# Optimization experiments

Measured on AMD Instinct MI355X. Metric: run time of the kernel, lower is better.

The kernel has to match this reference:

```python
import jax, jax.numpy as jnp
import numpy as np

ALPHA = 0.2          # LeakyReLU negative slope
NEG_INF = -9e15      # standard GAT masking constant


def gat_layer(h, adj_mask, W, a_src, a_dst):
    # h: [N, D], adj_mask: [N, N] bool
    Wh = h @ W                                  # [N, D]
    e = (Wh @ a_src)[:, None] + (Wh @ a_dst)[None, :]  # [N, N]
    e = jax.nn.leaky_relu(e, negative_slope=ALPHA)
    e = jnp.where(adj_mask, e, NEG_INF)
    attn = jax.nn.softmax(e, axis=-1)           # [N, N]
    return jax.nn.relu(attn @ Wh)               # PlainGCN applies ReLU


def setup_inputs() -> dict:
    key = jax.random.key(0)
    ks = jax.random.split(key, 8)
    N, D = 8192, 256
    x = jax.random.normal(ks[0], (N, D), dtype=jnp.float32)
    adj = jax.random.randint(ks[1], (N, N), 0, 2, dtype=jnp.int32)
    s = 1.0 / np.sqrt(D)
    W1 = jax.random.normal(ks[2], (D, D), dtype=jnp.float32) * s
    a1_src = jax.random.normal(ks[3], (D,), dtype=jnp.float32) * s
    a1_dst = jax.random.normal(ks[4], (D,), dtype=jnp.float32) * s
    W2 = jax.random.normal(ks[5], (D, D), dtype=jnp.float32) * s
    a2_src = jax.random.normal(ks[6], (D,), dtype=jnp.float32) * s
    a2_dst = jax.random.normal(ks[7], (D,), dtype=jnp.float32) * s
    return {"x": x, "adj": adj, "W1": W1, "a1_src": a1_src, "a1_dst": a1_dst,
            "W2": W2, "a2_src": a2_src, "a2_dst": a2_dst}


def reference(x, adj, W1, a1_src, a1_dst, W2, a2_src, a2_dst):
    adj_mask = adj > 0
    h = gat_layer(x, adj_mask, W1, a1_src, a1_dst)
    h = gat_layer(h, adj_mask, W2, a2_src, a2_dst)
    return h
```

## Files before the change

kernel.cpp:

```cpp
#include <hip/hip_runtime.h>
#include <cstdint>
#include <cstddef>


#define ALPHA 0.2f
#define NN 8192
#define DD 256

typedef __attribute__((ext_vector_type(8))) short short8;
typedef __attribute__((ext_vector_type(4))) float f32x4;
typedef __attribute__((ext_vector_type(2))) _Float16 half2v;
typedef __attribute__((ext_vector_type(8))) __fp16 h8;

__device__ __forceinline__ unsigned pk_f16(float a, float b) {
    return __builtin_bit_cast(unsigned, __builtin_amdgcn_cvt_pkrtz(a, b));
}

__device__ __forceinline__ int sbit(uint32_t x, int o) {
    return ((int)(x << (31 - o))) >> 31;
}

__device__ __forceinline__ uint32_t hmerge(uint32_t hi, uint32_t lo) {
#if __has_builtin(__builtin_amdgcn_perm)
    return __builtin_amdgcn_perm(hi, lo, 0x07060100u);
#else
    return (hi & 0xFFFF0000u) | (lo & 0x0000FFFFu);
#endif
}

__device__ __forceinline__ half2v pkmax(half2v a, half2v b) {
#if __has_builtin(__builtin_elementwise_max)
    return __builtin_elementwise_max(a, b);
#else
    half2v r;
    asm("v_pk_max_f16 %0, %1, %2" : "=v"(r) : "v"(a), "v"(b));
    return r;
#endif
}

__device__ __forceinline__ f32x4 mfma_f16(uint4 a, short8 b, f32x4 c) {
    return __builtin_amdgcn_mfma_f32_16x16x32_f16(__builtin_bit_cast(h8, a),
                                                  __builtin_bit_cast(h8, b), c, 0, 0, 0);
}


__device__ __forceinline__ void packbits_dev(const int* __restrict__ adj,
                                             uint64_t* __restrict__ bits,
                                             int row, int lane) {
    const int* rowp = adj + (size_t)row * NN;
    uint64_t* dst = bits + (size_t)row * 128;
    for (int it = 0; it < 16; it++) {
        const int* p = rowp + it * 512;
        int a0 = p[lane];
        int a1 = p[64 + lane];
        int a2 = p[128 + lane];
        int a3 = p[192 + lane];
        int a4 = p[256 + lane];
        int a5 = p[320 + lane];
        int a6 = p[384 + lane];
        int a7 = p[448 + lane];
        uint64_t m0 = __ballot(a0 != 0);
        uint64_t m1 = __ballot(a1 != 0);
        uint64_t m2 = __ballot(a2 != 0);
        uint64_t m3 = __ballot(a3 != 0);
        uint64_t m4 = __ballot(a4 != 0);
        uint64_t m5 = __ballot(a5 != 0);
        uint64_t m6 = __ballot(a6 != 0);
        uint64_t m7 = __ballot(a7 != 0);
        if (lane == 0) {
            dst[it * 8 + 0] = m0; dst[it * 8 + 1] = m1;
            dst[it * 8 + 2] = m2; dst[it * 8 + 3] = m3;
            dst[it * 8 + 4] = m4; dst[it * 8 + 5] = m5;
            dst[it * 8 + 6] = m6; dst[it * 8 + 7] = m7;
        }
    }
}

__device__ __forceinline__ void transp_dev(const uint32_t* __restrict__ bits32,
                                           uint32_t* __restrict__ bitsT,
                                           int job, unsigned char* smem, int t) {
    uint32_t (*tile)[65] = (uint32_t (*)[65])smem;
    const int i0 = (job >> 2) * 64;
    const int w0 = (job & 3) * 64;
#pragma unroll
    for (int p = 0; p < 4; p++) {
        int r = (t >> 4) + 16 * p;
        int c4 = (t & 15) * 4;
        uint4 v = *(const uint4*)(bits32 + (size_t)(i0 + r) * 256 + w0 + c4);
        tile[r][c4 + 0] = v.x; tile[r][c4 + 1] = v.y;
        tile[r][c4 + 2] = v.z; tile[r][c4 + 3] = v.w;
    }
    __syncthreads();
#pragma unroll
    for (int p = 0; p < 4; p++) {
        int wr = (t >> 4) + 16 * p;
        int i4 = (t & 15) * 4;
        uint4 o = {tile[i4][wr], tile[i4 + 1][wr], tile[i4 + 2][wr], tile[i4 + 3][wr]};
        *(uint4*)(bitsT + (size_t)(w0 + wr) * NN + i0 + i4) = o;
    }
}

__device__ __forceinline__ void gemm_dev(const float* __restrict__ A,
                                         const float* __restrict__ B,
                                         unsigned short* __restrict__ Bpack,
                                         const float* __restrict__ a_src,
                                         const float* __restrict__ a_dst,
                                         float* __restrict__ s4,
                                         float* __restrict__ dd4,
                                         int job, unsigned char* smem, int t) {
    float (*At)[36] = (float (*)[36])smem;
    float2 (*Bs)[32] = (float2 (*)[32])(smem + 4608);
    const int m0 = (job >> 2) * 32;
    const int cq = job & 3;
    const int r0 = (t >> 5) * 4;
    const int cl = t & 31;
    float acc[4][2];
#pragma unroll
    for (int i = 0; i < 4; i++) { acc[i][0] = 0.f; acc[i][1] = 0.f; }

    for (int k0 = 0; k0 < DD; k0 += 32) {
        {
            int row = t >> 3, kq = t & 7;
            float4 v = *(const float4*)(A + (size_t)(m0 + row) * DD + k0 + kq * 4);
            At[kq * 4 + 0][row] = v.x; At[kq * 4 + 1][row] = v.y;
            At[kq * 4 + 2][row] = v.z; At[kq * 4 + 3][row] = v.w;
        }
#pragma unroll
        for (int l2 = 0; l2 < 2; l2++) {
            int fi = l2 * 256 + t;
            int br = fi >> 4, bc4 = fi & 15;
            float4 v = *(const float4*)(B + (size_t)(k0 + br) * DD + cq * 64 + bc4 * 4);
            Bs[br][bc4 * 2] = {v.x, v.y};
            Bs[br][bc4 * 2 + 1] = {v.z, v.w};
        }
        __syncthreads();
#pragma unroll
        for (int k = 0; k < 32; k++) {
            float4 a0 = *(const float4*)&At[k][r0];
            float2 b = Bs[k][cl];
            float av[4] = {a0.x, a0.y, a0.z, a0.w};
#pragma unroll
            for (int i = 0; i < 4; i++) {
                acc[i][0] += av[i] * b.x;
                acc[i][1] += av[i] * b.y;
            }
        }
        __syncthreads();
    }

    const int jt = m0 >> 5;
    const int lq = ((r0 >> 3) & 3) * 16;
    const int i8 = r0 & 4;
#pragma unroll
    for (int cc = 0; cc < 2; cc++) {
        int c = cq * 64 + cl * 2 + cc;
        int ct = c >> 4;
        int lane = lq + (c & 15);
        uint2 pk;
        pk.x = pk_f16(acc[0][cc], acc[1][cc]);
        pk.y = pk_f16(acc[2][cc], acc[3][cc]);
        *(uint2*)(Bpack + ((size_t)(jt * 16 + ct) * 64 + lane) * 8 + i8) = pk;
    }

    const int c0 = cq * 64 + cl * 2;
    float as0 = a_src[c0], as1 = a_src[c0 + 1];
    float ad0 = a_dst[c0], ad1 = a_dst[c0 + 1];
    float ps[4], pd[4];
#pragma unroll
    for (int i = 0; i < 4; i++) {
        ps[i] = acc[i][0] * as0 + acc[i][1] * as1;
        pd[i] = acc[i][0] * ad0 + acc[i][1] * ad1;
    }
#pragma unroll
    for (int off = 16; off; off >>= 1) {
#pragma unroll
        for (int i = 0; i < 4; i++) {
            ps[i] += __shfl_xor(ps[i], off);
            pd[i] += __shfl_xor(pd[i], off);
        }
    }
    if (cl == 0) {
#pragma unroll
        for (int i = 0; i < 4; i++) {
            s4[(size_t)cq * NN + m0 + r0 + i] = ps[i];
            dd4[(size_t)cq * NN + m0 + r0 + i] = pd[i];
        }
    }
}

__device__ __forceinline__ void fhgen_dev(const float* __restrict__ s4,
                                          const float* __restrict__ dd4,
                                          float* __restrict__ s,
                                          uint32_t* __restrict__ FF,
                                          uint32_t* __restrict__ HH,
                                          float* __restrict__ dmax32,
                                          int job, float* sred, int t) {
    const int i = job * 256 + t;
    float ssum = (s4[i] + s4[i + NN]) + (s4[i + 2 * NN] + s4[i + 3 * NN]);
    float dsum = (dd4[i] + dd4[i + NN]) + (dd4[i + 2 * NN] + dd4[i + 3 * NN]);
    s[i] = ssum;
    float F = __expf(dsum);
    float H = __expf(ALPHA * dsum);
    float Fn = __shfl_xor(F, 1);
    float Hn = __shfl_xor(H, 1);
    if ((i & 1) == 0) {
        FF[i >> 1] = pk_f16(F, Fn);
        HH[i >> 1] = pk_f16(H, Hn);
    }
    float bm = dsum;
#pragma unroll
    for (int off = 32; off; off >>= 1) bm = fmaxf(bm, __shfl_xor(bm, off));
    const int wave = t >> 6, lane = t & 63;
    if (lane == 0) sred[wave] = bm;
    __syncthreads();
    if (t == 0) dmax32[job] = fmaxf(fmaxf(sred[0], sred[1]), fmaxf(sred[2], sred[3]));
}


__global__ __launch_bounds__(256) void mega1(const float* __restrict__ A,
                                             const float* __restrict__ W,
                                             unsigned short* __restrict__ Bpack,
                                             const float* __restrict__ a_src,
                                             const float* __restrict__ a_dst,
                                             float* __restrict__ s4,
                                             float* __restrict__ dd4,
                                             const int* __restrict__ adj,
                                             uint64_t* __restrict__ bits) {
    __shared__ __align__(16) unsigned char smem[12800];
    const int bx = blockIdx.x;
    const int t = threadIdx.x;
    const int sel = bx % 3;
    const int base = bx / 3;
    if (sel == 0) {
        gemm_dev(A, W, Bpack, a_src, a_dst, s4, dd4, base, smem, t);
    } else {
        const int row = base * 8 + (sel - 1) * 4 + (t >> 6);
        packbits_dev(adj, bits, row, t & 63);
    }
}

__global__ __launch_bounds__(256) void megaB(const uint32_t* __restrict__ bits32,
                                             uint32_t* __restrict__ bitsT,
                                             const float* __restrict__ s4,
                                             const float* __restrict__ dd4,
                                             float* __restrict__ s,
                                             uint32_t* __restrict__ FF,
                                             uint32_t* __restrict__ HH,
                                             float* __restrict__ dmax32) {
    __shared__ __align__(16) unsigned char smem[16640];
    const int bx = blockIdx.x;
    const int t = threadIdx.x;
    if (bx < 512) {
        transp_dev(bits32, bitsT, bx, smem, t);
    } else {
        fhgen_dev(s4, dd4, s, FF, HH, dmax32, bx - 512, (float*)smem, t);
    }
}

__global__ __launch_bounds__(256) void k_gemm(const float* A, const float* W,
                                              unsigned short* Bpack,
                                              const float* a_src, const float* a_dst,
                                              float* s4, float* dd4) {
    __shared__ __align__(16) unsigned char smem[12800];
    gemm_dev(A, W, Bpack, a_src, a_dst, s4, dd4, blockIdx.x, smem, threadIdx.x);
}
__global__ __launch_bounds__(256) void k_fhgen(const float* __restrict__ s4,
                                               const float* __restrict__ dd4,
                                               float* __restrict__ s,
                                               uint32_t* __restrict__ FF,
                                               uint32_t* __restrict__ HH,
                                               float* __restrict__ dmax32) {
    __shared__ float sred[4];
    fhgen_dev(s4, dd4, s, FF, HH, dmax32, blockIdx.x, sred, threadIdx.x);
}

__global__ __launch_bounds__(256) void epgen(const float* __restrict__ s,
                                             const float* __restrict__ dmax32,
                                             float* __restrict__ Ep,
                                             float* __restrict__ Gp) {
    __shared__ float sm;
    const int t = threadIdx.x;
    if (t == 0) {
        float m = dmax32[0];
#pragma unroll
        for (int k = 1; k < 32; k++) m = fmaxf(m, dmax32[k]);
        sm = m;
    }
    __syncthreads();
    const float dmax = sm;
    const int i = blockIdx.x * 256 + t;
    float si = s[i];
    float e = si + dmax;
    float m = e >= 0.f ? e : ALPHA * e;
    Ep[i] = 256.0f * __expf(si - m);
    Gp[i] = 256.0f * __expf(ALPHA * si - m);
}

__global__ __launch_bounds__(256, 4) void pv_mfma(const unsigned short* __restrict__ Bpack,
                                                  const uint32_t* __restrict__ bitsT,
                                                  const uint32_t* __restrict__ FF,
                                                  const uint32_t* __restrict__ HH,
                                                  const float* __restrict__ Ep,
                                                  const float* __restrict__ Gp,
                                                  float* __restrict__ pout,
                                                  float* __restrict__ rsum) {
    __shared__ __align__(16) uint4 pb[2][256];
    __shared__ __align__(16) uint32_t sFF[512];
    __shared__ __align__(16) uint32_t sHH[512];
    const int t = threadIdx.x;
    const int w = t >> 6, l = t & 63;
    const int bx = blockIdx.x;
    const int ks = bx & 7;
    const int i0 = (bx >> 3) * 64;
    const int kbase = ks * 32;

    const int rl16 = l & 15;
    const int ko = (l >> 4) * 8;
    const int fo = ko >> 1;
    const int rw = i0 + 16 * w + rl16;
    const _Float16 eph = (_Float16)Ep[rw];
    const _Float16 gph = (_Float16)Gp[rw];
    const half2v ep2 = {eph, eph};
    const half2v gp2 = {gph, gph};

    const unsigned short* bb = Bpack + ((size_t)(w * 4) * 64 + l) * 8;
    const uint32_t* btb = bitsT + rw;

    if (t < 128) {
        ((uint4*)sFF)[t] = *(const uint4*)(FF + kbase * 16 + t * 4);
    } else {
        ((uint4*)sHH)[t - 128] = *(const uint4*)(HH + kbase * 16 + (t - 128) * 4);
    }

    f32x4 acc[4][4];
#pragma unroll
    for (int i = 0; i < 4; i++)
#pragma unroll
        for (int q = 0; q < 4; q++) acc[i][q] = (f32x4){0.f, 0.f, 0.f, 0.f};
    float rsv = 0.f;

    auto build = [&](int jl, uint32_t bw) -> uint4 {
        uint4 fw = *(const uint4*)(sFF + jl * 16 + fo);
        uint4 hw = *(const uint4*)(sHH + jl * 16 + fo);
        const uint32_t fwa[4] = {fw.x, fw.y, fw.z, fw.w};
        const uint32_t hwa[4] = {hw.x, hw.y, hw.z, hw.w};
        const uint32_t wl = bw >> ko;
        uint32_t au[4];
#pragma unroll
        for (int p = 0; p < 4; p++) {
            half2v f2 = __builtin_bit_cast(half2v, fwa[p]);
            half2v h2 = __builtin_bit_cast(half2v, hwa[p]);
            half2v pm = ep2 * f2;
            half2v pa = gp2 * h2;
            half2v px = pkmax(pm, pa);
            uint32_t mlo = (uint32_t)sbit(wl, 2 * p);
            uint32_t mhi = (uint32_t)sbit(wl, 2 * p + 1);
            au[p] = __builtin_bit_cast(uint32_t, px) & hmerge(mhi, mlo);
        }
        half2v s01 = __builtin_bit_cast(half2v, au[0]) + __builtin_bit_cast(half2v, au[1]);
        half2v s23 = __builtin_bit_cast(half2v, au[2]) + __builtin_bit_cast(half2v, au[3]);
        half2v sp = s01 + s23;
        rsv += (float)sp.x + (float)sp.y;
        return (uint4){au[0], au[1], au[2], au[3]};
    };

    uint32_t bwc = btb[(size_t)kbase * NN];
    __syncthreads();

    uint4 aucur = build(0, bwc);
    pb[0][w * 64 + l] = aucur;
    uint32_t bwn = btb[(size_t)(kbase + 1) * NN];

    for (int jl = 0; jl < 32; jl++) {
        const int par = jl & 1;
        const unsigned short* bp = bb + (size_t)(kbase + jl) * 8192;
        short8 B0 = *(const short8*)(bp);
        short8 B1 = *(const short8*)(bp + 512);
        short8 B2 = *(const short8*)(bp + 1024);
        short8 B3 = *(const short8*)(bp + 1536);

        __syncthreads();

#pragma unroll
        for (int f = 0; f < 4; f++) {
            uint4 af;
            if (f == w) af = aucur;
            else        af = pb[par][f * 64 + l];
            acc[f][0] = mfma_f16(af, B0, acc[f][0]);
            acc[f][1] = mfma_f16(af, B1, acc[f][1]);
            acc[f][2] = mfma_f16(af, B2, acc[f][2]);
            acc[f][3] = mfma_f16(af, B3, acc[f][3]);
        }

        if (jl < 31) {
            uint4 an = build(jl + 1, bwn);
            pb[par ^ 1][w * 64 + l] = an;
            aucur = an;
            if (jl < 30) bwn = btb[(size_t)(kbase + jl + 2) * NN];
        }
    }

    rsv += __shfl_xor(rsv, 16);
    rsv += __shfl_xor(rsv, 32);
    if (l < 16) rsum[(size_t)ks * NN + rw] = rsv;

    float* outp = pout + (size_t)ks * NN * DD;
#pragma unroll
    for (int f = 0; f < 4; f++) {
        const int orow = i0 + 16 * f + (l >> 4) * 4;
#pragma unroll
        for (int q = 0; q < 4; q++) {
            const int ocol = w * 64 + q * 16 + rl16;
#pragma unroll
            for (int r = 0; r < 4; r++)
                outp[(size_t)(orow + r) * DD + ocol] = acc[f][q][r];
        }
    }
}

__global__ __launch_bounds__(256) void combine8(const float* __restrict__ p,
                                                const float* __restrict__ rsum,
                                                float* __restrict__ out) {
    const size_t S = (size_t)NN * DD / 4;
    size_t idx = (size_t)blockIdx.x * 256 + threadIdx.x;
    const int row = (int)(idx >> 6);
    float rs = (rsum[row] + rsum[row + NN]) + (rsum[row + 2 * NN] + rsum[row + 3 * NN])
             + (rsum[row + 4 * NN] + rsum[row + 5 * NN])
             + (rsum[row + 6 * NN] + rsum[row + 7 * NN]);
    const float inv = 1.0f / rs;
    float4 a0 = ((const float4*)p)[idx];
    float4 a1 = ((const float4*)p)[idx + S];
    float4 a2 = ((const float4*)p)[idx + 2 * S];
    float4 a3 = ((const float4*)p)[idx + 3 * S];
    float4 a4 = ((const float4*)p)[idx + 4 * S];
    float4 a5 = ((const float4*)p)[idx + 5 * S];
    float4 a6 = ((const float4*)p)[idx + 6 * S];
    float4 a7 = ((const float4*)p)[idx + 7 * S];
    float4 o;
    o.x = fmaxf((((a0.x + a1.x) + (a2.x + a3.x)) + ((a4.x + a5.x) + (a6.x + a7.x))) * inv, 0.f);
    o.y = fmaxf((((a0.y + a1.y) + (a2.y + a3.y)) + ((a4.y + a5.y) + (a6.y + a7.y))) * inv, 0.f);
    o.z = fmaxf((((a0.z + a1.z) + (a2.z + a3.z)) + ((a4.z + a5.z) + (a6.z + a7.z))) * inv, 0.f);
    o.w = fmaxf((((a0.w + a1.w) + (a2.w + a3.w)) + ((a4.w + a5.w) + (a6.w + a7.w))) * inv, 0.f);
    ((float4*)out)[idx] = o;
}

extern "C" void kernel_launch(void* const* d_in, const int* in_sizes, int n_in,
                              void* d_out, int out_size, void* d_ws, size_t ws_size,
                              hipStream_t stream) {
    const float* x   = (const float*)d_in[0];
    const int* adj   = (const int*)d_in[1];
    const float* W1  = (const float*)d_in[2];
    const float* a1s = (const float*)d_in[3];
    const float* a1d = (const float*)d_in[4];
    const float* W2  = (const float*)d_in[5];
    const float* a2s = (const float*)d_in[6];
    const float* a2d = (const float*)d_in[7];
    float* out = (float*)d_out;

    char* ws = (char*)d_ws;
    const size_t MB = 1024ull * 1024ull;
    uint64_t*       bits  = (uint64_t*)(ws + 8 * MB);
    uint32_t*       bits32= (uint32_t*)bits;
    uint32_t*       bitsT = (uint32_t*)(ws + 16 * MB);
    float*          sArr  = (float*)(ws + 24 * MB);
    float*          EpA   = sArr + NN;
    float*          GpA   = sArr + 2 * NN;
    float*          s4    = sArr + 3 * NN;
    float*          dd4   = sArr + 7 * NN;
    float*          rsumA = sArr + 11 * NN;
    uint32_t*       FFA   = (uint32_t*)(sArr + 19 * NN);
    uint32_t*       HHA   = FFA + NN / 2;
    float*          dmax32= sArr + 20 * NN;
    unsigned short* Bpack = (unsigned short*)(ws + 25 * MB);
    float*          pout  = (float*)(ws + 32 * MB);

    mega1<<<dim3(3072), dim3(256), 0, stream>>>(x, W1, Bpack, a1s, a1d, s4, dd4,
                                                adj, bits);
    megaB<<<dim3(544), dim3(256), 0, stream>>>(bits32, bitsT, s4, dd4, sArr,
                                               FFA, HHA, dmax32);
    epgen<<<dim3(32), dim3(256), 0, stream>>>(sArr, dmax32, EpA, GpA);
    pv_mfma<<<dim3(1024), dim3(256), 0, stream>>>(Bpack, bitsT, FFA, HHA, EpA, GpA,
                                                  pout, rsumA);
    combine8<<<dim3(2048), dim3(256), 0, stream>>>(pout, rsumA, out);

    k_gemm<<<dim3(1024), dim3(256), 0, stream>>>(out, W2, Bpack, a2s, a2d, s4, dd4);
    k_fhgen<<<dim3(32), dim3(256), 0, stream>>>(s4, dd4, sArr, FFA, HHA, dmax32);
    epgen<<<dim3(32), dim3(256), 0, stream>>>(sArr, dmax32, EpA, GpA);
    pv_mfma<<<dim3(1024), dim3(256), 0, stream>>>(Bpack, bitsT, FFA, HHA, EpA, GpA,
                                                  pout, rsumA);
    combine8<<<dim3(2048), dim3(256), 0, stream>>>(pout, rsumA, out);
}
```

Baseline: 517.7 us.

## Fold epgen into pv_mfma and halve the split-K partitions from eight to four

Removes the separate epgen kernel by having every pv_mfma wave reduce dmax32 with shuffles and compute its row's Ep/Gp scale factors inline. The split-K factor over the 256 column blocks drops from 8 to 4, so each block runs 64 iterations and there are 512 blocks. This halves the partial-output traffic written by pv_mfma and read by combine4, and removes two launches. The cost is half as many blocks, which lowers occupancy and parallelism, and a longer serial loop per block.

```diff
diff --git a/kernel.cpp b/kernel.cpp
--- a/kernel.cpp
+++ b/kernel.cpp
@@ -274,63 +274,45 @@
     fhgen_dev(s4, dd4, s, FF, HH, dmax32, blockIdx.x, sred, threadIdx.x);
 }
 
-__global__ __launch_bounds__(256) void epgen(const float* __restrict__ s,
-                                             const float* __restrict__ dmax32,
-                                             float* __restrict__ Ep,
-                                             float* __restrict__ Gp) {
-    __shared__ float sm;
-    const int t = threadIdx.x;
-    if (t == 0) {
-        float m = dmax32[0];
-#pragma unroll
-        for (int k = 1; k < 32; k++) m = fmaxf(m, dmax32[k]);
-        sm = m;
-    }
-    __syncthreads();
-    const float dmax = sm;
-    const int i = blockIdx.x * 256 + t;
-    float si = s[i];
-    float e = si + dmax;
-    float m = e >= 0.f ? e : ALPHA * e;
-    Ep[i] = 256.0f * __expf(si - m);
-    Gp[i] = 256.0f * __expf(ALPHA * si - m);
-}
-
 __global__ __launch_bounds__(256, 4) void pv_mfma(const unsigned short* __restrict__ Bpack,
                                                   const uint32_t* __restrict__ bitsT,
                                                   const uint32_t* __restrict__ FF,
                                                   const uint32_t* __restrict__ HH,
-                                                  const float* __restrict__ Ep,
-                                                  const float* __restrict__ Gp,
+                                                  const float* __restrict__ s,
+                                                  const float* __restrict__ dmax32,
                                                   float* __restrict__ pout,
                                                   float* __restrict__ rsum) {
     __shared__ __align__(16) uint4 pb[2][256];
-    __shared__ __align__(16) uint32_t sFF[512];
-    __shared__ __align__(16) uint32_t sHH[512];
+    __shared__ __align__(16) uint32_t sFF[1024];
+    __shared__ __align__(16) uint32_t sHH[1024];
     const int t = threadIdx.x;
     const int w = t >> 6, l = t & 63;
     const int bx = blockIdx.x;
-    const int ks = bx & 7;
-    const int i0 = (bx >> 3) * 64;
-    const int kbase = ks * 32;
+    const int ks = bx & 3;
+    const int i0 = (bx >> 2) * 64;
+    const int kbase = ks * 64;
 
     const int rl16 = l & 15;
     const int ko = (l >> 4) * 8;
     const int fo = ko >> 1;
     const int rw = i0 + 16 * w + rl16;
-    const _Float16 eph = (_Float16)Ep[rw];
-    const _Float16 gph = (_Float16)Gp[rw];
-    const half2v ep2 = {eph, eph};
-    const half2v gp2 = {gph, gph};
+
+    float dm = (l < 32) ? dmax32[l] : -3.0e38f;
+#pragma unroll
+    for (int off = 32; off; off >>= 1) dm = fmaxf(dm, __shfl_xor(dm, off));
+    const float si = s[rw];
+    const float e0 = si + dm;
+    const float m = e0 >= 0.f ? e0 : ALPHA * e0;
+    const float Eps = 256.0f * __expf(si - m);
+    const float Gps = 256.0f * __expf(ALPHA * si - m);
+    const half2v ep2 = {(_Float16)Eps, (_Float16)Eps};
+    const half2v gp2 = {(_Float16)Gps, (_Float16)Gps};
 
     const unsigned short* bb = Bpack + ((size_t)(w * 4) * 64 + l) * 8;
     const uint32_t* btb = bitsT + rw;
 
-    if (t < 128) {
-        ((uint4*)sFF)[t] = *(const uint4*)(FF + kbase * 16 + t * 4);
-    } else {
-        ((uint4*)sHH)[t - 128] = *(const uint4*)(HH + kbase * 16 + (t - 128) * 4);
-    }
+    ((uint4*)sFF)[t] = *(const uint4*)(FF + kbase * 16 + t * 4);
+    ((uint4*)sHH)[t] = *(const uint4*)(HH + kbase * 16 + t * 4);
 
     f32x4 acc[4][4];
 #pragma unroll
@@ -371,7 +353,7 @@
     pb[0][w * 64 + l] = aucur;
     uint32_t bwn = btb[(size_t)(kbase + 1) * NN];
 
-    for (int jl = 0; jl < 32; jl++) {
+    for (int jl = 0; jl < 64; jl++) {
         const int par = jl & 1;
         const unsigned short* bp = bb + (size_t)(kbase + jl) * 8192;
         short8 B0 = *(const short8*)(bp);
@@ -392,11 +374,11 @@
             acc[f][3] = mfma_f16(af, B3, acc[f][3]);
         }
 
-        if (jl < 31) {
+        if (jl < 63) {
             uint4 an = build(jl + 1, bwn);
             pb[par ^ 1][w * 64 + l] = an;
             aucur = an;
-            if (jl < 30) bwn = btb[(size_t)(kbase + jl + 2) * NN];
+            if (jl < 62) bwn = btb[(size_t)(kbase + jl + 2) * NN];
         }
     }
 
@@ -418,29 +400,23 @@
     }
 }
 
-__global__ __launch_bounds__(256) void combine8(const float* __restrict__ p,
+__global__ __launch_bounds__(256) void combine4(const float* __restrict__ p,
                                                 const float* __restrict__ rsum,
                                                 float* __restrict__ out) {
     const size_t S = (size_t)NN * DD / 4;
     size_t idx = (size_t)blockIdx.x * 256 + threadIdx.x;
     const int row = (int)(idx >> 6);
-    float rs = (rsum[row] + rsum[row + NN]) + (rsum[row + 2 * NN] + rsum[row + 3 * NN])
-             + (rsum[row + 4 * NN] + rsum[row + 5 * NN])
-             + (rsum[row + 6 * NN] + rsum[row + 7 * NN]);
+    float rs = (rsum[row] + rsum[row + NN]) + (rsum[row + 2 * NN] + rsum[row + 3 * NN]);
     const float inv = 1.0f / rs;
     float4 a0 = ((const float4*)p)[idx];
     float4 a1 = ((const float4*)p)[idx + S];
     float4 a2 = ((const float4*)p)[idx + 2 * S];
     float4 a3 = ((const float4*)p)[idx + 3 * S];
-    float4 a4 = ((const float4*)p)[idx + 4 * S];
-    float4 a5 = ((const float4*)p)[idx + 5 * S];
-    float4 a6 = ((const float4*)p)[idx + 6 * S];
-    float4 a7 = ((const float4*)p)[idx + 7 * S];
     float4 o;
-    o.x = fmaxf((((a0.x + a1.x) + (a2.x + a3.x)) + ((a4.x + a5.x) + (a6.x + a7.x))) * inv, 0.f);
-    o.y = fmaxf((((a0.y + a1.y) + (a2.y + a3.y)) + ((a4.y + a5.y) + (a6.y + a7.y))) * inv, 0.f);
-    o.z = fmaxf((((a0.z + a1.z) + (a2.z + a3.z)) + ((a4.z + a5.z) + (a6.z + a7.z))) * inv, 0.f);
-    o.w = fmaxf((((a0.w + a1.w) + (a2.w + a3.w)) + ((a4.w + a5.w) + (a6.w + a7.w))) * inv, 0.f);
+    o.x = fmaxf(((a0.x + a1.x) + (a2.x + a3.x)) * inv, 0.f);
+    o.y = fmaxf(((a0.y + a1.y) + (a2.y + a3.y)) * inv, 0.f);
+    o.z = fmaxf(((a0.z + a1.z) + (a2.z + a3.z)) * inv, 0.f);
+    o.w = fmaxf(((a0.w + a1.w) + (a2.w + a3.w)) * inv, 0.f);
     ((float4*)out)[idx] = o;
 }
 
@@ -463,14 +439,12 @@
     uint32_t*       bits32= (uint32_t*)bits;
     uint32_t*       bitsT = (uint32_t*)(ws + 16 * MB);
     float*          sArr  = (float*)(ws + 24 * MB);
-    float*          EpA   = sArr + NN;
-    float*          GpA   = sArr + 2 * NN;
-    float*          s4    = sArr + 3 * NN;
-    float*          dd4   = sArr + 7 * NN;
-    float*          rsumA = sArr + 11 * NN;
-    uint32_t*       FFA   = (uint32_t*)(sArr + 19 * NN);
+    float*          s4    = sArr + NN;
+    float*          dd4   = sArr + 5 * NN;
+    float*          rsumA = sArr + 9 * NN;
+    uint32_t*       FFA   = (uint32_t*)(sArr + 13 * NN);
     uint32_t*       HHA   = FFA + NN / 2;
-    float*          dmax32= sArr + 20 * NN;
+    float*          dmax32= sArr + 14 * NN;
     unsigned short* Bpack = (unsigned short*)(ws + 25 * MB);
     float*          pout  = (float*)(ws + 32 * MB);
 
@@ -478,15 +452,13 @@
                                                 adj, bits);
     megaB<<<dim3(544), dim3(256), 0, stream>>>(bits32, bitsT, s4, dd4, sArr,
                                                FFA, HHA, dmax32);
-    epgen<<<dim3(32), dim3(256), 0, stream>>>(sArr, dmax32, EpA, GpA);
-    pv_mfma<<<dim3(1024), dim3(256), 0, stream>>>(Bpack, bitsT, FFA, HHA, EpA, GpA,
-                                                  pout, rsumA);
-    combine8<<<dim3(2048), dim3(256), 0, stream>>>(pout, rsumA, out);
+    pv_mfma<<<dim3(512), dim3(256), 0, stream>>>(Bpack, bitsT, FFA, HHA, sArr,
+                                                 dmax32, pout, rsumA);
+    combine4<<<dim3(2048), dim3(256), 0, stream>>>(pout, rsumA, out);
 
     k_gemm<<<dim3(1024), dim3(256), 0, stream>>>(out, W2, Bpack, a2s, a2d, s4, dd4);
     k_fhgen<<<dim3(32), dim3(256), 0, stream>>>(s4, dd4, sArr, FFA, HHA, dmax32);
-    epgen<<<dim3(32), dim3(256), 0, stream>>>(sArr, dmax32, EpA, GpA);
-    pv_mfma<<<dim3(1024), dim3(256), 0, stream>>>(Bpack, bitsT, FFA, HHA, EpA, GpA,
-                                                  pout, rsumA);
-    combine8<<<dim3(2048), dim3(256), 0, stream>>>(pout, rsumA, out);
-}
+    pv_mfma<<<dim3(512), dim3(256), 0, stream>>>(Bpack, bitsT, FFA, HHA, sArr,
+                                                 dmax32, pout, rsumA);
+    combine4<<<dim3(2048), dim3(256), 0, stream>>>(pout, rsumA, out);
+}
```

Result: no change. 515.0 us (-0.5%).
